# Optimization experiments

Hardware: AMD Instinct MI355X
Metric: run time of the kernel (lower is better)

Reference implementation:

```python
import jax, jax.numpy as jnp
import numpy as np

B, L, D = 8, 8192, 512
TARGET_RATIO = 1.0 / 6.0


def _normalize(v):
    # matches torch F.normalize(dim=-1, eps=1e-12)
    n = jnp.maximum(jnp.linalg.norm(v, axis=-1, keepdims=True), 1e-12)
    return v / n


def _downsample(x, b_hard):
    # vectorized stream compaction, padded to L (static upper bound of L_max)
    Bb, Ll, Dd = x.shape
    cnt = jnp.cumsum(b_hard.astype(jnp.int32), axis=1)
    pos = jnp.where(b_hard > 0.5, cnt - 1, Ll)          # non-selected -> dump slot L
    bidx = jnp.arange(Bb)[:, None]
    out = jnp.zeros((Bb, Ll + 1, Dd), x.dtype).at[bidx, pos].set(x)[:, :Ll]
    counts = cnt[:, -1]
    mask = jnp.arange(Ll)[None, :] < counts[:, None]
    return out, mask


def setup_inputs() -> dict:
    key = jax.random.key(0)
    k1, k2, k3 = jax.random.split(key, 3)
    x = jax.random.normal(k1, (B, L, D), jnp.float32)
    W_q = jax.random.normal(k2, (D, D), jnp.float32) / np.sqrt(D)
    W_k = jax.random.normal(k3, (D, D), jnp.float32) / np.sqrt(D)
    return {"x": x, "W_q": W_q, "W_k": W_k}


def reference(x, W_q, W_k):
    q = _normalize(jnp.einsum('bld,ed->ble', x, W_q))   # nn.Linear: x @ W.T
    k = _normalize(jnp.einsum('bld,ed->ble', x, W_k))
    k_prev = jnp.pad(k[:, :-1, :], ((0, 0), (1, 0), (0, 0)))
    cos_sim = jnp.sum(q * k_prev, axis=-1)               # (B, L)
    p = jnp.clip(0.5 * (1.0 - cos_sim), 0.0, 1.0)
    p = p.at[:, 0].set(1.0)                              # first position always boundary
    b_hard = (p >= 0.5).astype(x.dtype)
    N = 1.0 / TARGET_RATIO
    F_actual = jnp.mean(b_hard)
    G_actual = jnp.mean(p)
    ratio_loss = N / (N - 1.0) * ((N - 1.0) * F_actual * G_actual + (1.0 - F_actual) * (1.0 - G_actual))
    compressed, comp_mask = _downsample(x, b_hard)
    p_compressed, _ = _downsample(p[..., None], b_hard)
    p_compressed = p_compressed[..., 0]
    return (compressed, comp_mask, b_hard, p, p_compressed, ratio_loss)
```

## Files before the change

kernel.cpp:

```cpp
#include <hip/hip_runtime.h>
#include <hip/hip_bf16.h>
#include <math.h>

#define BB 8
#define LL 8192
#define DD 512
#define NROWS (BB * LL)

#define OUT_COMP   0
#define OUT_MASK   33554432
#define OUT_BHARD  33619968
#define OUT_P      33685504
#define OUT_PCOMP  33751040
#define OUT_LOSS   33816576

#define WS_FIXLIST 0
#define WS_FIXCNT  262144
#define WS_COUNTS  262148
#define WS_SUMP    262180
#define WS_SEL     262212
#define WS_SSK     524416
#define WS_SSQ     786560
#define WS_DOT     1048704
#define WS_WQH     1310848
#define WS_WKH     1835136

#define FIX_CAP 65536
#define FIX_TAU 5e-5f

typedef __attribute__((ext_vector_type(8))) _Float16 half8;
typedef __attribute__((ext_vector_type(4))) float f32x4;

static __device__ __forceinline__ void ld_g2l16(const void* g, void* l) {
  __builtin_amdgcn_global_load_lds(
      (const __attribute__((address_space(1))) void*)g,
      (__attribute__((address_space(3))) void*)l, 16, 0, 0);
}

__global__ __launch_bounds__(256) void wsplit(
    const float* __restrict__ Wq, const float* __restrict__ Wk,
    _Float16* __restrict__ wqh, _Float16* __restrict__ wkh,
    float* __restrict__ ssk, float* __restrict__ ssq,
    float* __restrict__ dotb, int* __restrict__ fixcnt) {
  const int t = blockIdx.x * 256 + threadIdx.x;
  if (t == 0) *fixcnt = 0;
  ssk[t] = 0.0f;
  ssq[t] = 0.0f;
  dotb[t] = 0.0f;

  const int m = t >> 15;
  const int c = t & 32767;
  const int kt = c >> 11;
  const int ct = (c >> 6) & 31;
  const int l = c & 63;
  const int n = l & 15;
  const int kblk = l >> 4;
  const int e = ct * 16 + n;
  const int d0 = kt * 32 + kblk * 8;
  const float* src = (m ? Wk : Wq) + (long)e * 512 + d0;
  _Float16* dh = (m ? wkh : wqh) + (long)c * 8;
  float4 v0 = *(const float4*)src;
  float4 v1 = *(const float4*)(src + 4);
  float av[8] = {v0.x, v0.y, v0.z, v0.w, v1.x, v1.y, v1.z, v1.w};
  half8 hi;
#pragma unroll
  for (int j = 0; j < 8; ++j) hi[j] = (_Float16)av[j];
  *(half8*)dh = hi;
}

__global__ __launch_bounds__(256, 2) void gemm_fused(
    const float* __restrict__ x,
    const _Float16* __restrict__ wqh, const _Float16* __restrict__ wkh,
    float* __restrict__ ssqOut, float* __restrict__ sskOut,
    float* __restrict__ dotOut,
    float* __restrict__ qedge, float* __restrict__ kedge) {
  __shared__ float smemf[8704];
  float* A0 = smemf;
  float* A1 = smemf + 4096;

  const int tid = threadIdx.x;
  const int lane = tid & 63;
  const int w = tid >> 6;
  const int wrow = w & 1, wcol = w >> 1;
  const int g = lane >> 4, n = lane & 15;
  const int bx0 = blockIdx.x;
  const int bx = ((bx0 & 7) << 8) | (bx0 >> 3);
  const int rb = bx >> 2, cb = bx & 3;
  const long r0 = (long)rb * 128;

  const int srow = w * 32 + (lane >> 3);
  const int scol = (((lane & 7) ^ (lane >> 3)) << 2);
  const float* gsrc = x + (r0 + srow) * 512 + scol;

  const int sw = (lane & 7) << 4;
  const int kb0 = (lane >> 4) << 5;
  const int o1 = kb0 ^ sw;
  const int o2 = (kb0 + 16) ^ sw;
  const int rdrow0 = wrow * 64 + (lane & 15);

  const _Float16* bqb = wqh + ((long)((cb * 8 + wcol * 4) * 64 + lane)) * 8;
  const _Float16* bkb = wkh + ((long)((cb * 8 + wcol * 4) * 64 + lane)) * 8;

  f32x4 accq[4][4], acck[4][4];
#pragma unroll
  for (int mb = 0; mb < 4; ++mb)
#pragma unroll
    for (int nb = 0; nb < 4; ++nb) {
      accq[mb][nb] = (f32x4){0.f, 0.f, 0.f, 0.f};
      acck[mb][nb] = (f32x4){0.f, 0.f, 0.f, 0.f};
    }

  half8 bq[4], bk[4];

#define STAGE_A(ktv, AB_)                                                 \
  do {                                                                    \
    _Pragma("unroll") for (int j = 0; j < 4; ++j)                         \
        ld_g2l16(gsrc + j * 4096 + (ktv) * 32,                            \
                 (char*)(AB_) + (w * 4 + j) * 1024);                      \
  } while (0)

#define LOAD_B_ALL(ktv)                                                   \
  do {                                                                    \
    _Pragma("unroll") for (int nb = 0; nb < 4; ++nb) {                    \
      bq[nb] = *(const half8*)(bqb + (long)(ktv)*16384 + nb * 512);       \
      bk[nb] = *(const half8*)(bkb + (long)(ktv)*16384 + nb * 512);       \
    }                                                                     \
  } while (0)

#define COMPUTE(AB_, KTN)                                                 \
  do {                                                                    \
    half8 ah[4], al[4];                                                   \
    _Pragma("unroll") for (int mb = 0; mb < 4; ++mb) {                    \
      const char* rp = (const char*)((AB_) + (rdrow0 + mb * 16) * 32);    \
      float4 v0 = *(const float4*)(rp + o1);                              \
      float4 v1 = *(const float4*)(rp + o2);                              \
      float av[8] = {v0.x, v0.y, v0.z, v0.w, v1.x, v1.y, v1.z, v1.w};     \
      half8 h, lo;                                                        \
      _Pragma("unroll") for (int j = 0; j < 8; ++j) {                     \
        _Float16 a = (_Float16)av[j];                                     \
        h[j] = a;                                                         \
        lo[j] = (_Float16)(av[j] - (float)a);                             \
      }                                                                   \
      ah[mb] = h;                                                         \
      al[mb] = lo;                                                        \
    }                                                                     \
    _Pragma("unroll") for (int nb = 0; nb < 4; ++nb) {                    \
      __builtin_amdgcn_s_setprio(1);                                      \
      _Pragma("unroll") for (int mb = 0; mb < 4; ++mb) {                  \
        accq[mb][nb] = __builtin_amdgcn_mfma_f32_16x16x32_f16(            \
            ah[mb], bq[nb], accq[mb][nb], 0, 0, 0);                       \
        acck[mb][nb] = __builtin_amdgcn_mfma_f32_16x16x32_f16(            \
            ah[mb], bk[nb], acck[mb][nb], 0, 0, 0);                       \
        accq[mb][nb] = __builtin_amdgcn_mfma_f32_16x16x32_f16(            \
            al[mb], bq[nb], accq[mb][nb], 0, 0, 0);                       \
        acck[mb][nb] = __builtin_amdgcn_mfma_f32_16x16x32_f16(            \
            al[mb], bk[nb], acck[mb][nb], 0, 0, 0);                       \
      }                                                                   \
      __builtin_amdgcn_s_setprio(0);                                      \
      bq[nb] = *(const half8*)(bqb + (long)(KTN)*16384 + nb * 512);       \
      bk[nb] = *(const half8*)(bkb + (long)(KTN)*16384 + nb * 512);       \
    }                                                                     \
  } while (0)

#define BARRIER_CNT()                                       \
  do {                                                      \
    asm volatile("s_waitcnt vmcnt(8)" ::: "memory");        \
    asm volatile("s_waitcnt lgkmcnt(0)" ::: "memory");      \
    __builtin_amdgcn_sched_barrier(0);                      \
    __builtin_amdgcn_s_barrier();                           \
  } while (0)

#define FENCE() __builtin_amdgcn_sched_barrier(0)

  STAGE_A(0, A0);
  FENCE();
  LOAD_B_ALL(0);
  FENCE();
  BARRIER_CNT();

  for (int i = 0; i < 8; ++i) {
    const int kt = 2 * i;
    STAGE_A(kt + 1, A1);
    FENCE();
    COMPUTE(A0, kt + 1);
    BARRIER_CNT();
    {
      const int ktn = (kt + 2 < 16) ? (kt + 2) : 15;
      STAGE_A(ktn, A0);
      FENCE();
      COMPUTE(A1, ktn);
    }
    BARRIER_CNT();
  }

  asm volatile("s_waitcnt vmcnt(0)" ::: "memory");
  __builtin_amdgcn_sched_barrier(0);
  __syncthreads();

  _Float16* KX = (_Float16*)smemf;
  const int col0 = wcol * 64 + n;
  const int rbase = wrow * 64;
#pragma unroll
  for (int mb = 0; mb < 4; ++mb)
#pragma unroll
    for (int reg = 0; reg < 4; ++reg) {
      const int rl = rbase + mb * 16 + g * 4 + reg;
#pragma unroll
      for (int nb = 0; nb < 4; ++nb)
        KX[rl * 136 + col0 + nb * 16] = (_Float16)acck[mb][nb][reg];
    }
  __syncthreads();

  if (wrow == 1 && g == 3) {
#pragma unroll
    for (int nb = 0; nb < 4; ++nb)
      kedge[rb * 512 + cb * 128 + col0 + nb * 16] = acck[3][nb][3];
  }
  if (wrow == 0 && g == 0) {
#pragma unroll
    for (int nb = 0; nb < 4; ++nb)
      qedge[rb * 512 + cb * 128 + col0 + nb * 16] = accq[0][nb][0];
  }

#pragma unroll
  for (int mb = 0; mb < 4; ++mb) {
#pragma unroll
    for (int reg = 0; reg < 4; ++reg) {
      const int rl = rbase + mb * 16 + g * 4 + reg;
      const long row = r0 + rl;
      float sq = 0.f, sk = 0.f, dt = 0.f;
#pragma unroll
      for (int nb = 0; nb < 4; ++nb) {
        float qv = accq[mb][nb][reg];
        float kv = acck[mb][nb][reg];
        sq = fmaf(qv, qv, sq);
        sk = fmaf(kv, kv, sk);
        if (rl > 0) {
          float kp = (float)KX[(rl - 1) * 136 + col0 + nb * 16];
          dt = fmaf(qv, kp, dt);
        }
      }
#pragma unroll
      for (int m = 1; m < 16; m <<= 1) {
        sq += __shfl_xor(sq, m, 64);
        sk += __shfl_xor(sk, m, 64);
        dt += __shfl_xor(dt, m, 64);
      }
      if (n == 0) {
        atomicAdd(&ssqOut[row], sq);
        atomicAdd(&sskOut[row], sk);
        if (rl > 0) atomicAdd(&dotOut[row], dt);
      }
    }
  }
#undef STAGE_A
#undef LOAD_B_ALL
#undef COMPUTE
#undef BARRIER_CNT
#undef FENCE
}

__global__ __launch_bounds__(64) void edgedot(
    const float* __restrict__ qedge, const float* __restrict__ kedge,
    float* __restrict__ dotOut) {
  const int rb = blockIdx.x;
  if (rb == 0) return;
  const long row = (long)rb * 128;
  if ((row & (LL - 1)) == 0) return;
  const int lane = threadIdx.x;
  float dt = 0.f;
#pragma unroll
  for (int c = lane; c < 512; c += 64)
    dt = fmaf(qedge[rb * 512 + c], kedge[(rb - 1) * 512 + c], dt);
#pragma unroll
  for (int m = 1; m < 64; m <<= 1) dt += __shfl_xor(dt, m, 64);
  if (lane == 0) dotOut[row] = dt;
}

__global__ __launch_bounds__(256) void combine(
    const float* __restrict__ ssq, const float* __restrict__ ssk,
    const float* __restrict__ dotb, float* __restrict__ dout,
    int* __restrict__ fixlist, int* __restrict__ fixcnt) {
  const int r = blockIdx.x * 256 + threadIdx.x;
  const int l = r & (LL - 1);
  float p;
  float cosv = 0.0f;
  if (l != 0) {
    float nq = fmaxf(sqrtf(ssq[r]), 1e-12f);
    float nk = fmaxf(sqrtf(ssk[r - 1]), 1e-12f);
    cosv = dotb[r] / (nq * nk);
    p = fminf(fmaxf(0.5f * (1.0f - cosv), 0.0f), 1.0f);
  } else {
    p = 1.0f;
  }
  dout[OUT_P + r] = p;
  dout[OUT_BHARD + r] = (p >= 0.5f) ? 1.0f : 0.0f;
  if (l != 0 && fabsf(cosv) < FIX_TAU) {
    int idx = atomicAdd(fixcnt, 1);
    if (idx < FIX_CAP) fixlist[idx] = r;
  }
}

__global__ __launch_bounds__(256) void fixup(
    const float* __restrict__ x, const float* __restrict__ Wq,
    const float* __restrict__ Wk, float* __restrict__ dout,
    const int* __restrict__ fixlist, const int* __restrict__ fixcnt) {
  __shared__ float xr[512], xp[512];
  __shared__ double red[3][256];
  const int t = threadIdx.x;
  int nfix = *fixcnt;
  if (nfix > FIX_CAP) nfix = FIX_CAP;

  for (int idx = blockIdx.x; idx < nfix; idx += gridDim.x) {
    const int r = fixlist[idx];
    for (int d = t; d < 512; d += 256) {
      xr[d] = x[(long)r * 512 + d];
      xp[d] = x[(long)(r - 1) * 512 + d];
    }
    __syncthreads();
    double ssq = 0.0, ssk = 0.0, dot = 0.0;
    for (int e = t; e < 512; e += 256) {
      const float* wq = Wq + (long)e * 512;
      const float* wk = Wk + (long)e * 512;
      double q = 0.0, k = 0.0;
      for (int d = 0; d < 512; ++d) {
        q = fma((double)xr[d], (double)wq[d], q);
        k = fma((double)xp[d], (double)wk[d], k);
      }
      ssq += q * q;
      ssk += k * k;
      dot += q * k;
    }
    red[0][t] = ssq;
    red[1][t] = ssk;
    red[2][t] = dot;
    __syncthreads();
    for (int s = 128; s > 0; s >>= 1) {
      if (t < s) {
        red[0][t] += red[0][t + s];
        red[1][t] += red[1][t + s];
        red[2][t] += red[2][t + s];
      }
      __syncthreads();
    }
    if (t == 0) {
      double nq = sqrt(red[0][0]);
      double nk = sqrt(red[1][0]);
      if (nq < 1e-12) nq = 1e-12;
      if (nk < 1e-12) nk = 1e-12;
      float c = (float)(red[2][0] / (nq * nk));
      float p = fminf(fmaxf(0.5f * (1.0f - c), 0.0f), 1.0f);
      dout[OUT_P + r] = p;
      dout[OUT_BHARD + r] = (p >= 0.5f) ? 1.0f : 0.0f;
    }
    __syncthreads();
  }
}

__global__ __launch_bounds__(256) void scanb(
    float* __restrict__ dout, int* __restrict__ sel,
    int* __restrict__ counts, float* __restrict__ sump) {
  __shared__ int wtot[4];
  __shared__ float wps[4];
  const int b = blockIdx.x;
  const int t = threadIdx.x;
  const int lane = t & 63, wv = t >> 6;
  const long base = (long)b * LL;

  int cnt = 0;
  float psum = 0.0f;
#pragma unroll 4
  for (int j = 0; j < 32; ++j) {
    int l = t * 32 + j;
    float bh = dout[OUT_BHARD + base + l];
    float pv = dout[OUT_P + base + l];
    cnt += (bh > 0.5f) ? 1 : 0;
    psum += pv;
  }
  int inc = cnt;
#pragma unroll
  for (int off = 1; off < 64; off <<= 1) {
    int u = __shfl_up(inc, off, 64);
    if (lane >= off) inc += u;
  }
  float ps = psum;
#pragma unroll
  for (int off = 1; off < 64; off <<= 1) ps += __shfl_xor(ps, off, 64);
  if (lane == 63) wtot[wv] = inc;
  if (lane == 0) wps[wv] = ps;
  __syncthreads();
  int wbase = 0, total = 0;
#pragma unroll
  for (int i = 0; i < 4; ++i) {
    int c = wtot[i];
    if (i < wv) wbase += c;
    total += c;
  }
  if (t == 0) {
    counts[b] = total;
    sump[b] = wps[0] + wps[1] + wps[2] + wps[3];
  }
  for (int j = 0; j < 32; ++j) {
    int l = t * 32 + j;
    dout[OUT_MASK + base + l] = (l < total) ? 1.0f : 0.0f;
    dout[OUT_PCOMP + base + l] = 0.0f;
  }
  __syncthreads();
  int pos = wbase + inc - cnt;
  for (int j = 0; j < 32; ++j) {
    int l = t * 32 + j;
    float bh = dout[OUT_BHARD + base + l];
    if (bh > 0.5f) {
      dout[OUT_PCOMP + base + pos] = dout[OUT_P + base + l];
      sel[base + pos] = l;
      ++pos;
    }
  }
}

__global__ void lossk(float* __restrict__ dout, const int* __restrict__ counts,
                      const float* __restrict__ sump) {
  if (threadIdx.x == 0 && blockIdx.x == 0) {
    float fc = 0.0f, gs = 0.0f;
    for (int b = 0; b < BB; ++b) {
      fc += (float)counts[b];
      gs += sump[b];
    }
    float F = fc / (float)NROWS;
    float G = gs / (float)NROWS;
    dout[OUT_LOSS] = 1.2f * (5.0f * F * G + (1.0f - F) * (1.0f - G));
  }
}

__global__ __launch_bounds__(128) void emit(
    const float* __restrict__ x, float* __restrict__ dout,
    const int* __restrict__ sel, const int* __restrict__ counts) {
  const long bid = blockIdx.x;
  const int b = (int)(bid >> 13);
  const int j = (int)(bid & (LL - 1));
  const int cnt = counts[b];
  float4 v = make_float4(0.0f, 0.0f, 0.0f, 0.0f);
  if (j < cnt) {
    const int l = sel[((long)b << 13) + j];
    v = *(const float4*)(x + (((long)b << 13) + l) * 512 + threadIdx.x * 4);
  }
  *(float4*)(dout + OUT_COMP + (((long)b << 13) + j) * 512 + threadIdx.x * 4) = v;
}

extern "C" void kernel_launch(void* const* d_in, const int* in_sizes, int n_in,
                              void* d_out, int out_size, void* d_ws,
                              size_t ws_size, hipStream_t stream) {
  const float* x = (const float*)d_in[0];
  const float* Wq = (const float*)d_in[1];
  const float* Wk = (const float*)d_in[2];
  float* out = (float*)d_out;
  char* ws = (char*)d_ws;

  int* fixlist = (int*)(ws + WS_FIXLIST);
  int* fixcnt = (int*)(ws + WS_FIXCNT);
  int* counts = (int*)(ws + WS_COUNTS);
  float* sump = (float*)(ws + WS_SUMP);
  int* sel = (int*)(ws + WS_SEL);
  float* ssk = (float*)(ws + WS_SSK);
  float* ssq = (float*)(ws + WS_SSQ);
  float* dotb = (float*)(ws + WS_DOT);
  _Float16* wqh = (_Float16*)(ws + WS_WQH);
  _Float16* wkh = (_Float16*)(ws + WS_WKH);

  float* kedge = (float*)(out + OUT_COMP);
  float* qedge = (float*)(out + OUT_COMP + 262144);

  wsplit<<<256, 256, 0, stream>>>(Wq, Wk, wqh, wkh, ssk, ssq, dotb, fixcnt);
  gemm_fused<<<2048, 256, 0, stream>>>(x, wqh, wkh, ssq, ssk, dotb, qedge, kedge);
  edgedot<<<512, 64, 0, stream>>>(qedge, kedge, dotb);
  combine<<<NROWS / 256, 256, 0, stream>>>(ssq, ssk, dotb, out, fixlist, fixcnt);
  fixup<<<512, 256, 0, stream>>>(x, Wq, Wk, out, fixlist, fixcnt);
  scanb<<<BB, 256, 0, stream>>>(out, sel, counts, sump);
  lossk<<<1, 64, 0, stream>>>(out, counts, sump);
  emit<<<NROWS, 128, 0, stream>>>(x, out, sel, counts);
}
```

Before: 457.2 us.

## Drop split-fp16 low term in GEMM, widen fixup band, restructure pipeline and fixup

The fused GEMM stops splitting x into fp16 high and low parts and issues half as many MFMAs, using a single fp16 rounding of x. It also stages two k-tiles per LDS buffer with double-buffered B registers. To keep boundary decisions exact, the fp64 fixup threshold is tripled so more near-zero cosine rows get recomputed. The fixup kernel now uses wave-level coalesced dot products with shuffle reductions instead of per-thread serial loops. The risk is lower GEMM precision, which may flip decisions outside the widened band, and more rows sent to the fixup pass.

After: 447.1 us. 2.2% less time.

```diff
diff --git a/kernel.cpp b/kernel.cpp
--- a/kernel.cpp
+++ b/kernel.cpp
@@ -26,7 +26,7 @@
 #define WS_WKH     1835136
 
 #define FIX_CAP 65536
-#define FIX_TAU 5e-5f
+#define FIX_TAU 1.5e-4f
 
 typedef __attribute__((ext_vector_type(8))) _Float16 half8;
 typedef __attribute__((ext_vector_type(4))) float f32x4;
@@ -74,9 +74,9 @@
     float* __restrict__ ssqOut, float* __restrict__ sskOut,
     float* __restrict__ dotOut,
     float* __restrict__ qedge, float* __restrict__ kedge) {
-  __shared__ float smemf[8704];
+  __shared__ float smemf[16384];
   float* A0 = smemf;
-  float* A1 = smemf + 4096;
+  float* A1 = smemf + 8192;
 
   const int tid = threadIdx.x;
   const int lane = tid & 63;
@@ -89,8 +89,8 @@
   const long r0 = (long)rb * 128;
 
   const int srow = w * 32 + (lane >> 3);
-  const int scol = (((lane & 7) ^ (lane >> 3)) << 2);
-  const float* gsrc = x + (r0 + srow) * 512 + scol;
+  const int scol = ((lane & 7) ^ (lane >> 3)) << 2;
+  const float* gsrc0 = x + (r0 + srow) * 512 + scol;
 
   const int sw = (lane & 7) << 4;
   const int kb0 = (lane >> 4) << 5;
@@ -110,61 +110,53 @@
       acck[mb][nb] = (f32x4){0.f, 0.f, 0.f, 0.f};
     }
 
-  half8 bq[4], bk[4];
-
-#define STAGE_A(ktv, AB_)                                                 \
+  half8 bq0[4], bk0[4], bq1[4], bk1[4];
+
+#define STAGE_A(pv, BUF)                                                  \
   do {                                                                    \
-    _Pragma("unroll") for (int j = 0; j < 4; ++j)                         \
-        ld_g2l16(gsrc + j * 4096 + (ktv) * 32,                            \
-                 (char*)(AB_) + (w * 4 + j) * 1024);                      \
+    _Pragma("unroll") for (int j = 0; j < 8; ++j) {                       \
+      const int ktp_ = j >> 2, jj_ = j & 3;                               \
+      ld_g2l16(gsrc0 + (long)jj_ * 8 * 512 + (pv)*64 + ktp_ * 32,         \
+               (char*)(BUF) + ktp_ * 16384 + (w * 4 + jj_) * 1024);       \
+    }                                                                     \
   } while (0)
 
-#define LOAD_B_ALL(ktv)                                                   \
+#define LOAD_B(BQ_, BK_, ktv)                                             \
   do {                                                                    \
     _Pragma("unroll") for (int nb = 0; nb < 4; ++nb) {                    \
-      bq[nb] = *(const half8*)(bqb + (long)(ktv)*16384 + nb * 512);       \
-      bk[nb] = *(const half8*)(bkb + (long)(ktv)*16384 + nb * 512);       \
+      BQ_[nb] = *(const half8*)(bqb + (long)(ktv)*16384 + nb * 512);      \
+      BK_[nb] = *(const half8*)(bkb + (long)(ktv)*16384 + nb * 512);      \
     }                                                                     \
   } while (0)
 
-#define COMPUTE(AB_, KTN)                                                 \
+#define COMPUTE(BUF, KTP, BQ_, BK_, KTN)                                  \
   do {                                                                    \
-    half8 ah[4], al[4];                                                   \
+    half8 ah[4];                                                          \
     _Pragma("unroll") for (int mb = 0; mb < 4; ++mb) {                    \
-      const char* rp = (const char*)((AB_) + (rdrow0 + mb * 16) * 32);    \
+      const char* rp =                                                    \
+          (const char*)((BUF) + (KTP)*4096 + (rdrow0 + mb * 16) * 32);    \
       float4 v0 = *(const float4*)(rp + o1);                              \
       float4 v1 = *(const float4*)(rp + o2);                              \
       float av[8] = {v0.x, v0.y, v0.z, v0.w, v1.x, v1.y, v1.z, v1.w};     \
-      half8 h, lo;                                                        \
-      _Pragma("unroll") for (int j = 0; j < 8; ++j) {                     \
-        _Float16 a = (_Float16)av[j];                                     \
-        h[j] = a;                                                         \
-        lo[j] = (_Float16)(av[j] - (float)a);                             \
-      }                                                                   \
+      half8 h;                                                            \
+      _Pragma("unroll") for (int j = 0; j < 8; ++j) h[j] = (_Float16)av[j]; \
       ah[mb] = h;                                                         \
-      al[mb] = lo;                                                        \
     }                                                                     \
-    _Pragma("unroll") for (int nb = 0; nb < 4; ++nb) {                    \
-      __builtin_amdgcn_s_setprio(1);                                      \
-      _Pragma("unroll") for (int mb = 0; mb < 4; ++mb) {                  \
-        accq[mb][nb] = __builtin_amdgcn_mfma_f32_16x16x32_f16(            \
-            ah[mb], bq[nb], accq[mb][nb], 0, 0, 0);                       \
-        acck[mb][nb] = __builtin_amdgcn_mfma_f32_16x16x32_f16(            \
-            ah[mb], bk[nb], acck[mb][nb], 0, 0, 0);                       \
-        accq[mb][nb] = __builtin_amdgcn_mfma_f32_16x16x32_f16(            \
-            al[mb], bq[nb], accq[mb][nb], 0, 0, 0);                       \
-        acck[mb][nb] = __builtin_amdgcn_mfma_f32_16x16x32_f16(            \
-            al[mb], bk[nb], acck[mb][nb], 0, 0, 0);                       \
-      }                                                                   \
-      __builtin_amdgcn_s_setprio(0);                                      \
-      bq[nb] = *(const half8*)(bqb + (long)(KTN)*16384 + nb * 512);       \
-      bk[nb] = *(const half8*)(bkb + (long)(KTN)*16384 + nb * 512);       \
+    __builtin_amdgcn_s_setprio(1);                                        \
+    _Pragma("unroll") for (int nb = 0; nb < 4; ++nb)                      \
+        _Pragma("unroll") for (int mb = 0; mb < 4; ++mb) {                \
+      accq[mb][nb] = __builtin_amdgcn_mfma_f32_16x16x32_f16(              \
+          ah[mb], BQ_[nb], accq[mb][nb], 0, 0, 0);                        \
+      acck[mb][nb] = __builtin_amdgcn_mfma_f32_16x16x32_f16(              \
+          ah[mb], BK_[nb], acck[mb][nb], 0, 0, 0);                        \
     }                                                                     \
+    __builtin_amdgcn_s_setprio(0);                                        \
+    LOAD_B(BQ_, BK_, KTN);                                                \
   } while (0)
 
 #define BARRIER_CNT()                                       \
   do {                                                      \
-    asm volatile("s_waitcnt vmcnt(8)" ::: "memory");        \
+    asm volatile("s_waitcnt vmcnt(16)" ::: "memory");       \
     asm volatile("s_waitcnt lgkmcnt(0)" ::: "memory");      \
     __builtin_amdgcn_sched_barrier(0);                      \
     __builtin_amdgcn_s_barrier();                           \
@@ -174,28 +166,27 @@
 
   STAGE_A(0, A0);
   FENCE();
-  LOAD_B_ALL(0);
+  LOAD_B(bq0, bk0, 0);
+  LOAD_B(bq1, bk1, 1);
   FENCE();
   BARRIER_CNT();
 
-  for (int i = 0; i < 8; ++i) {
-    const int kt = 2 * i;
-    STAGE_A(kt + 1, A1);
-    FENCE();
-    COMPUTE(A0, kt + 1);
-    BARRIER_CNT();
-    {
-      const int ktn = (kt + 2 < 16) ? (kt + 2) : 15;
-      STAGE_A(ktn, A0);
+  {
+    float* cur = A0;
+    float* nxt = A1;
+    for (int p = 0; p < 8; ++p) {
+      if (p < 7) STAGE_A(p + 1, nxt);
       FENCE();
-      COMPUTE(A1, ktn);
-    }
-    BARRIER_CNT();
-  }
-
-  asm volatile("s_waitcnt vmcnt(0)" ::: "memory");
-  __builtin_amdgcn_sched_barrier(0);
-  __syncthreads();
+      const int ktn0 = (2 * p + 2 < 16) ? 2 * p + 2 : 15;
+      const int ktn1 = (2 * p + 3 < 16) ? 2 * p + 3 : 15;
+      COMPUTE(cur, 0, bq0, bk0, ktn0);
+      COMPUTE(cur, 1, bq1, bk1, ktn1);
+      BARRIER_CNT();
+      float* t = cur;
+      cur = nxt;
+      nxt = t;
+    }
+  }
 
   _Float16* KX = (_Float16*)smemf;
   const int col0 = wcol * 64 + n;
@@ -254,7 +245,7 @@
     }
   }
 #undef STAGE_A
-#undef LOAD_B_ALL
+#undef LOAD_B
 #undef COMPUTE
 #undef BARRIER_CNT
 #undef FENCE
@@ -306,8 +297,9 @@
     const float* __restrict__ Wk, float* __restrict__ dout,
     const int* __restrict__ fixlist, const int* __restrict__ fixcnt) {
   __shared__ float xr[512], xp[512];
-  __shared__ double red[3][256];
+  __shared__ double wacc[3][4];
   const int t = threadIdx.x;
+  const int lane = t & 63, wv = t >> 6;
   int nfix = *fixcnt;
   if (nfix > FIX_CAP) nfix = FIX_CAP;
 
@@ -319,36 +311,39 @@
     }
     __syncthreads();
     double ssq = 0.0, ssk = 0.0, dot = 0.0;
-    for (int e = t; e < 512; e += 256) {
-      const float* wq = Wq + (long)e * 512;
-      const float* wk = Wk + (long)e * 512;
+    for (int e = wv; e < 512; e += 4) {
+      const float* wq = Wq + (long)e * 512 + lane;
+      const float* wk = Wk + (long)e * 512 + lane;
       double q = 0.0, k = 0.0;
-      for (int d = 0; d < 512; ++d) {
-        q = fma((double)xr[d], (double)wq[d], q);
-        k = fma((double)xp[d], (double)wk[d], k);
+#pragma unroll
+      for (int j = 0; j < 8; ++j) {
+        q = fma((double)xr[lane + j * 64], (double)wq[j * 64], q);
+        k = fma((double)xp[lane + j * 64], (double)wk[j * 64], k);
+      }
+#pragma unroll
+      for (int m = 1; m < 64; m <<= 1) {
+        q += __shfl_xor(q, m, 64);
+        k += __shfl_xor(k, m, 64);
       }
       ssq += q * q;
       ssk += k * k;
       dot += q * k;
     }
-    red[0][t] = ssq;
-    red[1][t] = ssk;
-    red[2][t] = dot;
+    if (lane == 0) {
+      wacc[0][wv] = ssq;
+      wacc[1][wv] = ssk;
+      wacc[2][wv] = dot;
+    }
     __syncthreads();
-    for (int s = 128; s > 0; s >>= 1) {
-      if (t < s) {
-        red[0][t] += red[0][t + s];
-        red[1][t] += red[1][t + s];
-        red[2][t] += red[2][t + s];
-      }
-      __syncthreads();
-    }
     if (t == 0) {
-      double nq = sqrt(red[0][0]);
-      double nk = sqrt(red[1][0]);
+      double SQ = wacc[0][0] + wacc[0][1] + wacc[0][2] + wacc[0][3];
+      double SK = wacc[1][0] + wacc[1][1] + wacc[1][2] + wacc[1][3];
+      double DT = wacc[2][0] + wacc[2][1] + wacc[2][2] + wacc[2][3];
+      double nq = sqrt(SQ);
+      double nk = sqrt(SK);
       if (nq < 1e-12) nq = 1e-12;
       if (nk < 1e-12) nk = 1e-12;
-      float c = (float)(red[2][0] / (nq * nk));
+      float c = (float)(DT / (nq * nk));
       float p = fminf(fmaxf(0.5f * (1.0f - c), 0.0f), 1.0f);
       dout[OUT_P + r] = p;
       dout[OUT_BHARD + r] = (p >= 0.5f) ? 1.0f : 0.0f;
```
